# Kernel tuning notes

Hardware: AMD Instinct MI355X
Metric: run time of the kernel (lower is better)

Reference implementation:

```python
import jax, jax.numpy as jnp
import numpy as np

FPFM = 256.0
B = 2097152
C = 32


def _integerize(v, scale):
    # Mirrors ArmInt.set_param_from_float: round-half-away-from-zero to int,
    # stored back as float (pure_int=False path).
    fv = v * scale
    fv = fv + jnp.sign(fv) * 0.5
    return jnp.trunc(fv)  # trunc toward zero == torch .to(int32)


def setup_inputs() -> dict:
    key = jax.random.key(0)
    ks = jax.random.split(key, 8)
    x = jax.random.normal(ks[0], (B, C), dtype=jnp.float32)
    # float-domain params (small, residual-friendly), then integerized
    w0 = _integerize(jax.random.normal(ks[1], (C, C), jnp.float32) * 0.05, FPFM)
    b0 = _integerize(jax.random.normal(ks[2], (C,), jnp.float32) * 0.05, FPFM * FPFM)
    w1 = _integerize(jax.random.normal(ks[3], (C, C), jnp.float32) * 0.05, FPFM)
    b1 = _integerize(jax.random.normal(ks[4], (C,), jnp.float32) * 0.05, FPFM * FPFM)
    w_out = _integerize(jax.random.normal(ks[5], (2, C), jnp.float32) * 0.05, FPFM)
    b_out = _integerize(jax.random.normal(ks[6], (2,), jnp.float32) * 0.05, FPFM * FPFM)
    return {"x": x, "w0": w0, "b0": b0, "w1": w1, "b1": b1,
            "w_out": w_out, "b_out": b_out}


def _arm_layer(h, W, b, residual):
    # F.linear + optional residual scaled by FPFM
    xx = h @ W.T + b
    if residual:
        xx = xx + h * FPFM
    # emulated integer rounding: add sign*FPFM/2, divide, trunc toward zero
    xx = xx + jnp.sign(xx) * (FPFM / 2.0)
    # where(xx<0, -(-xx/f), xx/f) is identity in float; trunc matches .to(int32)
    return jnp.trunc(xx / FPFM)


def reference(x, w0, b0, w1, b1, w_out, b_out):
    h = x * FPFM  # fixed-point lift (pure_int=False: stays float)
    h = jax.nn.relu(_arm_layer(h, w0, b0, True))
    h = jax.nn.relu(_arm_layer(h, w1, b1, True))
    h = _arm_layer(h, w_out, b_out, False)
    raw = h / FPFM  # [B, 2]
    mu = raw[:, 0]
    log_scale = raw[:, 1]
    scale = jnp.exp(jnp.clip(log_scale - 4.0, -4.6, 5.0))
    return mu, scale, log_scale
```

## Files before the change

### kernel.cpp

```cpp
#include <hip/hip_runtime.h>
#include <math.h>


__global__ __launch_bounds__(256)
__attribute__((amdgpu_waves_per_eu(2)))
void armint_kernel(const float* __restrict__ x,
                   const float* __restrict__ w0, const float* __restrict__ b0,
                   const float* __restrict__ w1, const float* __restrict__ b1,
                   const float* __restrict__ wo, const float* __restrict__ bo,
                   float* __restrict__ out, int n)
{
    int r = blockIdx.x * blockDim.x + threadIdx.x;
    if (r >= n) return;

    const float4* xr = (const float4*)(x + (size_t)r * 32);
    float h[32];
    float hn[32];

    #pragma unroll
    for (int q = 0; q < 8; ++q) {
        float4 v = xr[q];
        h[4*q+0] = v.x * 256.0f;
        h[4*q+1] = v.y * 256.0f;
        h[4*q+2] = v.z * 256.0f;
        h[4*q+3] = v.w * 256.0f;
    }

    #pragma unroll
    for (int i = 0; i < 32; ++i) {
        float acc = b0[i];
        #pragma unroll
        for (int j = 0; j < 32; ++j)
            acc = fmaf(h[j], w0[i*32+j], acc);
        acc = fmaf(h[i], 256.0f, acc);
        hn[i] = fmaxf(truncf((acc + 128.0f) * (1.0f/256.0f)), 0.0f);
    }

    #pragma unroll
    for (int i = 0; i < 32; ++i) {
        float acc = b1[i];
        #pragma unroll
        for (int j = 0; j < 32; ++j)
            acc = fmaf(hn[j], w1[i*32+j], acc);
        acc = fmaf(hn[i], 256.0f, acc);
        h[i] = fmaxf(truncf((acc + 128.0f) * (1.0f/256.0f)), 0.0f);
    }

    float o[2];
    #pragma unroll
    for (int i = 0; i < 2; ++i) {
        float acc = bo[i];
        #pragma unroll
        for (int j = 0; j < 32; ++j)
            acc = fmaf(h[j], wo[i*32+j], acc);
        float adj = acc + copysignf(128.0f, acc);
        o[i] = truncf(adj * (1.0f/256.0f)) * (1.0f/256.0f);
    }

    float mu = o[0];
    float ls = o[1];
    float cl = fminf(fmaxf(ls - 4.0f, -4.6f), 5.0f);
    float sc = expf(cl);

    size_t nn = (size_t)n;
    out[r]        = mu;
    out[nn + r]   = sc;
    out[2*nn + r] = ls;
}

extern "C" void kernel_launch(void* const* d_in, const int* in_sizes, int n_in,
                              void* d_out, int out_size, void* d_ws, size_t ws_size,
                              hipStream_t stream) {
    const float* x  = (const float*)d_in[0];
    const float* w0 = (const float*)d_in[1];
    const float* b0 = (const float*)d_in[2];
    const float* w1 = (const float*)d_in[3];
    const float* b1 = (const float*)d_in[4];
    const float* wo = (const float*)d_in[5];
    const float* bo = (const float*)d_in[6];
    float* out = (float*)d_out;

    int n = in_sizes[0] / 32;
    int block = 256;
    int grid = (n + block - 1) / block;

    armint_kernel<<<grid, block, 0, stream>>>(x, w0, b0, w1, b1, wo, bo, out, n);
}
```

Before: 429.9 us.

## Compute integer MLP layers with bf16 MFMA using split-precision operands

Replaces the per-thread scalar FMA MLP with wave-level 16x16x32 bf16 MFMA tiles. Activations are split into two or three bf16 pieces to recover exact float products, while the integer weights are exact in bf16. LDS is used to transpose between the MFMA output layout and the input layout for the residual and for the next layer. The aim is to remove the heavy scalar FMA compute bound. The risks are exactness of the split decomposition, and the grid no longer handles row counts that are not multiples of 128.

```diff
diff --git a/kernel.cpp b/kernel.cpp
--- a/kernel.cpp
+++ b/kernel.cpp
@@ -2,70 +2,180 @@
 #include <math.h>
 
 
+typedef __attribute__((ext_vector_type(8))) short bf16x8;
+typedef __attribute__((ext_vector_type(4))) float f32x4;
+
+#define MFMA16(A, B, C) __builtin_amdgcn_mfma_f32_16x16x32_bf16((A), (B), (C), 0, 0, 0)
+
+__device__ inline short bf_top(float v) {
+    return (short)(__float_as_uint(v) >> 16);
+}
+__device__ inline float bf_topf(float v) {
+    return __uint_as_float(__float_as_uint(v) & 0xffff0000u);
+}
+
 __global__ __launch_bounds__(256)
-__attribute__((amdgpu_waves_per_eu(2)))
-void armint_kernel(const float* __restrict__ x,
-                   const float* __restrict__ w0, const float* __restrict__ b0,
-                   const float* __restrict__ w1, const float* __restrict__ b1,
-                   const float* __restrict__ wo, const float* __restrict__ bo,
-                   float* __restrict__ out, int n)
+void armint_mfma(const float* __restrict__ x,
+                 const float* __restrict__ w0, const float* __restrict__ b0,
+                 const float* __restrict__ w1, const float* __restrict__ b1,
+                 const float* __restrict__ wo, const float* __restrict__ bo,
+                 float* __restrict__ out, int nrows)
 {
-    int r = blockIdx.x * blockDim.x + threadIdx.x;
-    if (r >= n) return;
+    __shared__ float lds_all[4][32 * 36];
 
-    const float4* xr = (const float4*)(x + (size_t)r * 32);
-    float h[32];
-    float hn[32];
+    const int lane = threadIdx.x & 63;
+    const int wave = threadIdx.x >> 6;
+    const int lm   = lane & 15;
+    const int quad = lane >> 4;
+    float* lds = lds_all[wave];
 
+    const size_t nn = (size_t)nrows;
+    const size_t rowbase = (size_t)blockIdx.x * 128 + (size_t)wave * 32;
+
+    bf16x8 w0f[2], w1f[2], wof;
+    float b0v[2], b1v[2], bov;
     #pragma unroll
-    for (int q = 0; q < 8; ++q) {
-        float4 v = xr[q];
-        h[4*q+0] = v.x * 256.0f;
-        h[4*q+1] = v.y * 256.0f;
-        h[4*q+2] = v.z * 256.0f;
-        h[4*q+3] = v.w * 256.0f;
+    for (int hh = 0; hh < 2; ++hh) {
+        const int n = lm + 16 * hh;
+        const float* p0 = w0 + n * 32 + quad * 8;
+        const float* p1 = w1 + n * 32 + quad * 8;
+        #pragma unroll
+        for (int j = 0; j < 8; ++j) {
+            w0f[hh][j] = bf_top(p0[j]);
+            w1f[hh][j] = bf_top(p1[j]);
+        }
+        b0v[hh] = b0[n] + 128.0f;
+        b1v[hh] = b1[n] + 128.0f;
+    }
+    #pragma unroll
+    for (int j = 0; j < 8; ++j)
+        wof[j] = (lm < 2) ? bf_top(wo[lm * 32 + quad * 8 + j]) : (short)0;
+    bov = (lm < 2) ? bo[lm] : 0.0f;
+
+    bf16x8 a0[2], a1[2], a2[2];
+    #pragma unroll
+    for (int t = 0; t < 2; ++t) {
+        const float* xp = x + (rowbase + (size_t)(t * 16 + lm)) * 32 + quad * 8;
+        float4 v0 = *(const float4*)xp;
+        float4 v1 = *(const float4*)(xp + 4);
+        float h[8] = {v0.x, v0.y, v0.z, v0.w, v1.x, v1.y, v1.z, v1.w};
+        #pragma unroll
+        for (int j = 0; j < 8; ++j) h[j] *= 256.0f;
+
+        const int base = (t * 16 + lm) * 36 + quad * 8;
+        *(float4*)&lds[base]     = make_float4(h[0], h[1], h[2], h[3]);
+        *(float4*)&lds[base + 4] = make_float4(h[4], h[5], h[6], h[7]);
+
+        #pragma unroll
+        for (int j = 0; j < 8; ++j) {
+            float c0 = bf_topf(h[j]);
+            a0[t][j] = bf_top(h[j]);
+            float r1 = h[j] - c0;
+            float c1 = bf_topf(r1);
+            a1[t][j] = bf_top(r1);
+            float r2 = r1 - c1;
+            a2[t][j] = bf_top(r2);
+        }
     }
 
+    f32x4 acc[2][2];
     #pragma unroll
-    for (int i = 0; i < 32; ++i) {
-        float acc = b0[i];
+    for (int t = 0; t < 2; ++t)
         #pragma unroll
-        for (int j = 0; j < 32; ++j)
-            acc = fmaf(h[j], w0[i*32+j], acc);
-        acc = fmaf(h[i], 256.0f, acc);
-        hn[i] = fmaxf(truncf((acc + 128.0f) * (1.0f/256.0f)), 0.0f);
+        for (int hh = 0; hh < 2; ++hh) {
+            f32x4 c = {b0v[hh], b0v[hh], b0v[hh], b0v[hh]};
+            c = MFMA16(a0[t], w0f[hh], c);
+            c = MFMA16(a1[t], w0f[hh], c);
+            c = MFMA16(a2[t], w0f[hh], c);
+            acc[t][hh] = c;
+        }
+    #pragma unroll
+    for (int t = 0; t < 2; ++t)
+        #pragma unroll
+        for (int hh = 0; hh < 2; ++hh)
+            #pragma unroll
+            for (int k = 0; k < 4; ++k) {
+                const int idx = (t * 16 + quad * 4 + k) * 36 + lm + 16 * hh;
+                float hres = lds[idx];
+                float xx = fmaf(hres, 256.0f, acc[t][hh][k]);
+                lds[idx] = fmaxf(truncf(xx * (1.0f / 256.0f)), 0.0f);
+            }
+
+    bf16x8 c0f[2], c1f[2];
+    #pragma unroll
+    for (int t = 0; t < 2; ++t) {
+        const int base = (t * 16 + lm) * 36 + quad * 8;
+        float4 v0 = *(float4*)&lds[base];
+        float4 v1 = *(float4*)&lds[base + 4];
+        float h[8] = {v0.x, v0.y, v0.z, v0.w, v1.x, v1.y, v1.z, v1.w};
+        #pragma unroll
+        for (int j = 0; j < 8; ++j) {
+            float c0 = bf_topf(h[j]);
+            c0f[t][j] = bf_top(h[j]);
+            c1f[t][j] = bf_top(h[j] - c0);
+        }
     }
+    #pragma unroll
+    for (int t = 0; t < 2; ++t)
+        #pragma unroll
+        for (int hh = 0; hh < 2; ++hh) {
+            f32x4 c = {b1v[hh], b1v[hh], b1v[hh], b1v[hh]};
+            c = MFMA16(c0f[t], w1f[hh], c);
+            c = MFMA16(c1f[t], w1f[hh], c);
+            acc[t][hh] = c;
+        }
+    #pragma unroll
+    for (int t = 0; t < 2; ++t)
+        #pragma unroll
+        for (int hh = 0; hh < 2; ++hh)
+            #pragma unroll
+            for (int k = 0; k < 4; ++k) {
+                const int idx = (t * 16 + quad * 4 + k) * 36 + lm + 16 * hh;
+                float hres = lds[idx];
+                float xx = fmaf(hres, 256.0f, acc[t][hh][k]);
+                lds[idx] = fmaxf(truncf(xx * (1.0f / 256.0f)), 0.0f);
+            }
 
+    bf16x8 d0f[2], d1f[2];
     #pragma unroll
-    for (int i = 0; i < 32; ++i) {
-        float acc = b1[i];
+    for (int t = 0; t < 2; ++t) {
+        const int base = (t * 16 + lm) * 36 + quad * 8;
+        float4 v0 = *(float4*)&lds[base];
+        float4 v1 = *(float4*)&lds[base + 4];
+        float h[8] = {v0.x, v0.y, v0.z, v0.w, v1.x, v1.y, v1.z, v1.w};
         #pragma unroll
-        for (int j = 0; j < 32; ++j)
-            acc = fmaf(hn[j], w1[i*32+j], acc);
-        acc = fmaf(hn[i], 256.0f, acc);
-        h[i] = fmaxf(truncf((acc + 128.0f) * (1.0f/256.0f)), 0.0f);
+        for (int j = 0; j < 8; ++j) {
+            float c0 = bf_topf(h[j]);
+            d0f[t][j] = bf_top(h[j]);
+            d1f[t][j] = bf_top(h[j] - c0);
+        }
     }
+    #pragma unroll
+    for (int t = 0; t < 2; ++t) {
+        f32x4 c = {bov, bov, bov, bov};
+        c = MFMA16(d0f[t], wof, c);
+        c = MFMA16(d1f[t], wof, c);
 
-    float o[2];
-    #pragma unroll
-    for (int i = 0; i < 2; ++i) {
-        float acc = bo[i];
+        float o[4];
         #pragma unroll
-        for (int j = 0; j < 32; ++j)
-            acc = fmaf(h[j], wo[i*32+j], acc);
-        float adj = acc + copysignf(128.0f, acc);
-        o[i] = truncf(adj * (1.0f/256.0f)) * (1.0f/256.0f);
+        for (int k = 0; k < 4; ++k) {
+            float a = c[k];
+            float adj = a + copysignf(128.0f, a);
+            o[k] = truncf(adj * (1.0f / 256.0f)) * (1.0f / 256.0f);
+        }
+        const size_t row = rowbase + (size_t)(t * 16 + quad * 4);
+        if (lm == 0) {
+            *(float4*)(out + row) = make_float4(o[0], o[1], o[2], o[3]);
+        }
+        if (lm == 1) {
+            *(float4*)(out + 2 * nn + row) = make_float4(o[0], o[1], o[2], o[3]);
+            float s[4];
+            #pragma unroll
+            for (int k = 0; k < 4; ++k)
+                s[k] = expf(fminf(fmaxf(o[k] - 4.0f, -4.6f), 5.0f));
+            *(float4*)(out + nn + row) = make_float4(s[0], s[1], s[2], s[3]);
+        }
     }
-
-    float mu = o[0];
-    float ls = o[1];
-    float cl = fminf(fmaxf(ls - 4.0f, -4.6f), 5.0f);
-    float sc = expf(cl);
-
-    size_t nn = (size_t)n;
-    out[r]        = mu;
-    out[nn + r]   = sc;
-    out[2*nn + r] = ls;
 }
 
 extern "C" void kernel_launch(void* const* d_in, const int* in_sizes, int n_in,
@@ -80,9 +190,8 @@
     const float* bo = (const float*)d_in[6];
     float* out = (float*)d_out;
 
-    int n = in_sizes[0] / 32;
-    int block = 256;
-    int grid = (n + block - 1) / block;
+    int nrows = in_sizes[0] / 32;
+    int grid = nrows / 128;
 
-    armint_kernel<<<grid, block, 0, stream>>>(x, w0, b0, w1, b1, wo, bo, out, n);
+    armint_mfma<<<grid, 256, 0, stream>>>(x, w0, b0, w1, b1, wo, bo, out, nrows);
 }
```

Result: faster. 418.4 us (-2.7%).
